# Kernel optimization log

Hardware: AMD Instinct MI355X
Metric: run time of the kernel (lower is better)

The kernel has to match this reference:

```python
import jax, jax.numpy as jnp
import numpy as np

N, E, F_IN, HID, HEADS, OUT, G = 50000, 800000, 128, 64, 4, 10, 64
NEG_SLOPE = 0.2


def _glorot(key, shape):
    fan = shape[0] + shape[-1]
    lim = np.sqrt(6.0 / fan)
    return jax.random.uniform(key, shape, jnp.float32, -lim, lim)


def setup_inputs() -> dict:
    key = jax.random.key(0)
    ks = jax.random.split(key, 20)
    x = jax.random.normal(ks[0], (N, F_IN), jnp.float32)
    edge_index = jax.random.randint(ks[1], (2, E), 0, N, jnp.int64)
    batch = jnp.sort(jax.random.randint(ks[2], (N,), 0, G, jnp.int64))
    inp = {"x": x, "edge_index": edge_index, "batch": batch}
    # layer 1: in=F_IN, heads=HEADS, out=HID
    inp["W1"] = _glorot(ks[3], (F_IN, HEADS * HID))
    inp["b1"] = jnp.zeros((HEADS * HID,), jnp.float32)
    inp["as1"] = _glorot(ks[4], (HEADS, HID))
    inp["ad1"] = _glorot(ks[5], (HEADS, HID))
    # layer 2: in=HEADS*HID, heads=HEADS, out=HID
    inp["W2"] = _glorot(ks[6], (HEADS * HID, HEADS * HID))
    inp["b2"] = jnp.zeros((HEADS * HID,), jnp.float32)
    inp["as2"] = _glorot(ks[7], (HEADS, HID))
    inp["ad2"] = _glorot(ks[8], (HEADS, HID))
    # layer 3: in=HEADS*HID, heads=1, out=HID
    inp["W3"] = _glorot(ks[9], (HEADS * HID, HID))
    inp["b3"] = jnp.zeros((HID,), jnp.float32)
    inp["as3"] = _glorot(ks[10], (1, HID))
    inp["ad3"] = _glorot(ks[11], (1, HID))
    # MLP head [HID, HID, OUT]
    inp["Wm1"] = _glorot(ks[12], (HID, HID))
    inp["bm1"] = jnp.zeros((HID,), jnp.float32)
    inp["Wm2"] = _glorot(ks[13], (HID, OUT))
    inp["bm2"] = jnp.zeros((OUT,), jnp.float32)
    return inp


def _gat_layer(x, src, dst, W, b, att_src, att_dst):
    # x: [N, Fin]; att_*: [H, C]
    H, C = att_src.shape
    h = (x @ W).reshape(N, H, C)
    a_src = jnp.einsum("nhc,hc->nh", h, att_src)
    a_dst = jnp.einsum("nhc,hc->nh", h, att_dst)
    alpha = jax.nn.leaky_relu(a_src[src] + a_dst[dst], NEG_SLOPE)  # [E', H]
    amax = jax.ops.segment_max(alpha, dst, num_segments=N)
    alpha = jnp.exp(alpha - amax[dst])
    denom = jax.ops.segment_sum(alpha, dst, num_segments=N)
    alpha = alpha / (denom[dst] + 1e-16)
    msg = h[src] * alpha[:, :, None]  # [E', H, C]
    out = jax.ops.segment_sum(msg, dst, num_segments=N)  # [N, H, C]
    return out.reshape(N, H * C) + b


def reference(x, edge_index, batch, W1, b1, as1, ad1, W2, b2, as2, ad2, W3, b3, as3, ad3, Wm1, bm1, Wm2, bm2):
    # PyG GATConv adds self-loops by default
    loops = jnp.arange(N, dtype=edge_index.dtype)
    src = jnp.concatenate([edge_index[0], loops])
    dst = jnp.concatenate([edge_index[1], loops])
    h = jax.nn.relu(_gat_layer(x, src, dst, W1, b1, as1, ad1))
    h = jax.nn.relu(_gat_layer(h, src, dst, W2, b2, as2, ad2))
    h = jax.nn.relu(_gat_layer(h, src, dst, W3, b3, as3, ad3))
    pooled = jax.ops.segment_sum(h, batch, num_segments=G)  # [G, HID]
    hidden = jax.nn.relu(pooled @ Wm1 + bm1)
    return hidden @ Wm2 + bm2
```

## Files before the change

### kernel.cpp

```cpp
#include <hip/hip_runtime.h>
#include <hip/hip_bf16.h>

#define F_IN   128
#define HID    64
#define HEADS  4
#define OUTD   10
#define NGRP   64

typedef unsigned short u16;
typedef __attribute__((ext_vector_type(8))) short short8;
typedef __attribute__((ext_vector_type(4))) float f32x4;

__device__ __forceinline__ float atomAddF(float* p, float v) {
    return __hip_atomic_fetch_add(p, v, __ATOMIC_RELAXED, __HIP_MEMORY_SCOPE_AGENT);
}
__device__ __forceinline__ float lrelu(float f) { return f > 0.f ? f : 0.2f * f; }
__device__ __forceinline__ float b2f(u16 u) { return __uint_as_float(((unsigned)u) << 16); }
__device__ __forceinline__ u16 f2b(float f) {
    unsigned u = __float_as_uint(f);
    return (u16)((u + 0x7fffu + ((u >> 16) & 1u)) >> 16);
}
__device__ __forceinline__ unsigned fmono(float f) {
    unsigned u = __float_as_uint(f);
    return (u & 0x80000000u) ? ~u : (u | 0x80000000u);
}
__device__ __forceinline__ float funmono(unsigned u) {
    return __uint_as_float((u & 0x80000000u) ? (u & 0x7FFFFFFFu) : ~u);
}

__global__ __launch_bounds__(256) void conv_kernel(const float* __restrict__ in,
                                                   u16* __restrict__ out, int n4) {
    int i = blockIdx.x * 256 + threadIdx.x;
    if (i >= n4) return;
    float4 v = ((const float4*)in)[i];
    uint2 o;
    o.x = (unsigned)f2b(v.x) | ((unsigned)f2b(v.y) << 16);
    o.y = (unsigned)f2b(v.z) | ((unsigned)f2b(v.w) << 16);
    ((uint2*)out)[i] = o;
}

__global__ __launch_bounds__(256) void wtrans_kernel(const float* __restrict__ W,
                                                     u16* __restrict__ Wt, int K, int NC) {
    int i = blockIdx.x * 256 + threadIdx.x;
    if (i >= K * NC) return;
    int n = i / K, k = i - n * K;
    Wt[i] = f2b(W[(size_t)k * NC + n]);
}

template<int K, int NC>
__global__ __launch_bounds__(256) void gemm_bf16_kernel(const u16* __restrict__ A,
                                                        const u16* __restrict__ Bt,
                                                        u16* __restrict__ Hb, int nrows) {
    constexpr int LDA = 40;
    __shared__ u16 As[64][LDA];
    __shared__ u16 Bs[NC][LDA];
    int tid = threadIdx.x;
    int m0 = blockIdx.x * 64;
    int w = tid >> 6, l = tid & 63, lr = l & 15, lk = l >> 4;
    if constexpr (NC == 256) {
        f32x4 acc[4][4] = {};
        for (int k0 = 0; k0 < K; k0 += 32) {
            {
                int row = tid >> 2, ks = (tid & 3) * 8;
                int grow = m0 + row;
                short8 av = {};
                if (grow < nrows) av = *(const short8*)&A[(size_t)grow * K + k0 + ks];
                *(short8*)&As[row][ks] = av;
            }
            #pragma unroll
            for (int i = 0; i < 4; i++) {
                int col = (tid >> 2) + 64 * i;
                int ks = (tid & 3) * 8;
                *(short8*)&Bs[col][ks] = *(const short8*)&Bt[(size_t)col * K + k0 + ks];
            }
            __syncthreads();
            short8 a[4], b[4];
            #pragma unroll
            for (int mi = 0; mi < 4; mi++) a[mi] = *(const short8*)&As[16 * mi + lr][lk * 8];
            #pragma unroll
            for (int ni = 0; ni < 4; ni++) b[ni] = *(const short8*)&Bs[64 * w + 16 * ni + lr][lk * 8];
            #pragma unroll
            for (int mi = 0; mi < 4; mi++)
                #pragma unroll
                for (int ni = 0; ni < 4; ni++)
                    acc[mi][ni] = __builtin_amdgcn_mfma_f32_16x16x32_bf16(a[mi], b[ni], acc[mi][ni], 0, 0, 0);
            __syncthreads();
        }
        #pragma unroll
        for (int mi = 0; mi < 4; mi++) {
            #pragma unroll
            for (int j = 0; j < 4; j++) {
                int grow = m0 + 16 * mi + lk * 4 + j;
                if (grow < nrows) {
                    #pragma unroll
                    for (int ni = 0; ni < 4; ni++)
                        Hb[(size_t)grow * NC + 64 * w + 16 * ni + lr] = f2b(acc[mi][ni][j]);
                }
            }
        }
    } else {
        f32x4 acc[NC / 16] = {};
        for (int k0 = 0; k0 < K; k0 += 32) {
            {
                int row = tid >> 2, ks = (tid & 3) * 8;
                int grow = m0 + row;
                short8 av = {};
                if (grow < nrows) av = *(const short8*)&A[(size_t)grow * K + k0 + ks];
                *(short8*)&As[row][ks] = av;
            }
            {
                int col = tid >> 2;
                int ks = (tid & 3) * 8;
                if (col < NC) *(short8*)&Bs[col][ks] = *(const short8*)&Bt[(size_t)col * K + k0 + ks];
            }
            __syncthreads();
            short8 af = *(const short8*)&As[16 * w + lr][lk * 8];
            #pragma unroll
            for (int c = 0; c < NC / 16; c++) {
                short8 bf = *(const short8*)&Bs[c * 16 + lr][lk * 8];
                acc[c] = __builtin_amdgcn_mfma_f32_16x16x32_bf16(af, bf, acc[c], 0, 0, 0);
            }
            __syncthreads();
        }
        #pragma unroll
        for (int c = 0; c < NC / 16; c++) {
            #pragma unroll
            for (int j = 0; j < 4; j++) {
                int grow = m0 + 16 * w + lk * 4 + j;
                if (grow < nrows) Hb[(size_t)grow * NC + c * 16 + lr] = f2b(acc[c][j]);
            }
        }
    }
}

template<int HH>
__global__ __launch_bounds__(256) void att_kernel(const u16* __restrict__ Hm,
                                                  const float* __restrict__ as_,
                                                  const float* __restrict__ ad_,
                                                  float* __restrict__ a_src,
                                                  float* __restrict__ a_dst, int n_nodes) {
    int wave = (blockIdx.x * 256 + threadIdx.x) >> 6;
    int lane = threadIdx.x & 63;
    if (wave >= n_nodes) return;
    const u16* hrow = Hm + (size_t)wave * HH * 64;
    #pragma unroll
    for (int hh = 0; hh < HH; hh++) {
        float v = b2f(hrow[hh * 64 + lane]);
        float s = v * as_[hh * 64 + lane];
        float d = v * ad_[hh * 64 + lane];
        #pragma unroll
        for (int off = 32; off; off >>= 1) {
            s += __shfl_xor(s, off, 64);
            d += __shfl_xor(d, off, 64);
        }
        if (lane == 0) { a_src[wave * HH + hh] = s; a_dst[wave * HH + hh] = d; }
    }
}

template<int HH>
__global__ __launch_bounds__(256) void gmax_kernel(const float* __restrict__ a_src,
                                                   unsigned* __restrict__ gmaxu, int n_nodes) {
    float mx[HH];
    #pragma unroll
    for (int h = 0; h < HH; h++) mx[h] = -3.4e38f;
    for (int i = blockIdx.x * 256 + threadIdx.x; i < n_nodes; i += gridDim.x * 256) {
        #pragma unroll
        for (int h = 0; h < HH; h++) mx[h] = fmaxf(mx[h], a_src[i * HH + h]);
    }
    #pragma unroll
    for (int h = 0; h < HH; h++) {
        #pragma unroll
        for (int off = 32; off; off >>= 1) mx[h] = fmaxf(mx[h], __shfl_xor(mx[h], off, 64));
    }
    if ((threadIdx.x & 63) == 0) {
        #pragma unroll
        for (int h = 0; h < HH; h++) atomicMax(&gmaxu[h], fmono(mx[h]));
    }
}

__global__ void count_kernel(const int* __restrict__ ei, int* __restrict__ deg,
                             int E_, int n_nodes) {
    int e = blockIdx.x * 256 + threadIdx.x;
    int tot = E_ + n_nodes;
    if (e >= tot) return;
    int d = (e < E_) ? ei[E_ + e] : e - E_;
    atomicAdd(&deg[d], 1);
}

__global__ __launch_bounds__(256) void scan_reduce_kernel(const int* __restrict__ deg,
                                                          int* __restrict__ bsum, int n) {
    int i = blockIdx.x * 256 + threadIdx.x;
    int v = (i < n) ? deg[i] : 0;
    #pragma unroll
    for (int o = 32; o; o >>= 1) v += __shfl_xor(v, o, 64);
    __shared__ int ws[4];
    if ((threadIdx.x & 63) == 0) ws[threadIdx.x >> 6] = v;
    __syncthreads();
    if (threadIdx.x == 0) bsum[blockIdx.x] = ws[0] + ws[1] + ws[2] + ws[3];
}

__global__ __launch_bounds__(256) void scan_blocksums_kernel(int* __restrict__ bsum, int nb) {
    __shared__ int s[256];
    int t = threadIdx.x;
    int v = (t < nb) ? bsum[t] : 0;
    s[t] = v;
    __syncthreads();
    #pragma unroll
    for (int d = 1; d < 256; d <<= 1) {
        int x = (t >= d) ? s[t - d] : 0;
        __syncthreads();
        s[t] += x;
        __syncthreads();
    }
    if (t < nb) bsum[t] = s[t] - v;
}

__global__ __launch_bounds__(256) void scan_final_kernel(const int* __restrict__ deg,
                                                         const int* __restrict__ bsum,
                                                         int* __restrict__ off, int n) {
    __shared__ int s[256];
    int t = threadIdx.x;
    int i = blockIdx.x * 256 + t;
    int v = (i < n) ? deg[i] : 0;
    s[t] = v;
    __syncthreads();
    #pragma unroll
    for (int d = 1; d < 256; d <<= 1) {
        int x = (t >= d) ? s[t - d] : 0;
        __syncthreads();
        s[t] += x;
        __syncthreads();
    }
    int ex = s[t] - v + bsum[blockIdx.x];
    if (i < n) off[i] = ex;
    if (i == n - 1) off[n] = ex + v;
}

__global__ void fill_kernel(const int* __restrict__ ei, const int* __restrict__ off,
                            int* __restrict__ cursor, int* __restrict__ csr_src,
                            int E_, int n_nodes) {
    int e = blockIdx.x * 256 + threadIdx.x;
    int tot = E_ + n_nodes;
    if (e >= tot) return;
    int s, d;
    if (e < E_) { s = ei[e]; d = ei[E_ + e]; } else { s = d = e - E_; }
    int pos = atomicAdd(&cursor[d], 1);
    csr_src[off[d] + pos] = s;
}

template<int HH, int CPL, bool OUTF32>
__global__ __launch_bounds__(256) void gat_aggr_kernel(const int* __restrict__ off,
                                                       const int* __restrict__ csr_src,
                                                       const u16* __restrict__ Hb,
                                                       const float* __restrict__ a_src,
                                                       const float* __restrict__ a_dst,
                                                       const unsigned* __restrict__ gmaxu,
                                                       const float* __restrict__ bias,
                                                       u16* __restrict__ outb16,
                                                       float* __restrict__ outf32,
                                                       int n_nodes) {
    constexpr int HC = 64 * CPL;
    constexpr int GRP = 64 / HH;
    int d = blockIdx.x * 4 + (threadIdx.x >> 6);
    if (d >= n_nodes) return;
    int lane = threadIdx.x & 63;
    int hh = lane / GRP;
    int g = lane & (GRP - 1);
    int gb = lane & (64 - GRP);
    int o0 = off[d];
    int deg = off[d + 1] - o0;
    float adm = a_dst[d * HH + hh];
    float m = lrelu(funmono(gmaxu[hh]) + adm);

    float den = 0.f;
    float acc[CPL] = {};
    int j = 0;
    for (; j + 4 <= deg; j += 4) {
        int s0 = csr_src[o0 + j + 0];
        int s1 = csr_src[o0 + j + 1];
        int s2 = csr_src[o0 + j + 2];
        int s3 = csr_src[o0 + j + 3];
        int ssel = s3;
        if (g == 0) ssel = s0; else if (g == 1) ssel = s1; else if (g == 2) ssel = s2;
        float e = __expf(lrelu(a_src[ssel * HH + hh] + adm) - m);
        float e0 = __shfl(e, gb + 0, 64);
        float e1 = __shfl(e, gb + 1, 64);
        float e2 = __shfl(e, gb + 2, 64);
        float e3 = __shfl(e, gb + 3, 64);
        den += (e0 + e1) + (e2 + e3);
        if constexpr (CPL == 4) {
            uint2 h0 = *(const uint2*)&Hb[(size_t)s0 * HC + lane * 4];
            uint2 h1 = *(const uint2*)&Hb[(size_t)s1 * HC + lane * 4];
            uint2 h2 = *(const uint2*)&Hb[(size_t)s2 * HC + lane * 4];
            uint2 h3 = *(const uint2*)&Hb[(size_t)s3 * HC + lane * 4];
            acc[0] += e0 * __uint_as_float(h0.x << 16) + e1 * __uint_as_float(h1.x << 16)
                    + e2 * __uint_as_float(h2.x << 16) + e3 * __uint_as_float(h3.x << 16);
            acc[1] += e0 * __uint_as_float(h0.x & 0xffff0000u) + e1 * __uint_as_float(h1.x & 0xffff0000u)
                    + e2 * __uint_as_float(h2.x & 0xffff0000u) + e3 * __uint_as_float(h3.x & 0xffff0000u);
            acc[2] += e0 * __uint_as_float(h0.y << 16) + e1 * __uint_as_float(h1.y << 16)
                    + e2 * __uint_as_float(h2.y << 16) + e3 * __uint_as_float(h3.y << 16);
            acc[3] += e0 * __uint_as_float(h0.y & 0xffff0000u) + e1 * __uint_as_float(h1.y & 0xffff0000u)
                    + e2 * __uint_as_float(h2.y & 0xffff0000u) + e3 * __uint_as_float(h3.y & 0xffff0000u);
        } else {
            u16 h0 = Hb[(size_t)s0 * HC + lane];
            u16 h1 = Hb[(size_t)s1 * HC + lane];
            u16 h2 = Hb[(size_t)s2 * HC + lane];
            u16 h3 = Hb[(size_t)s3 * HC + lane];
            acc[0] += e0 * b2f(h0) + e1 * b2f(h1) + e2 * b2f(h2) + e3 * b2f(h3);
        }
    }
    for (; j < deg; j++) {
        int s = csr_src[o0 + j];
        float al = __expf(lrelu(a_src[s * HH + hh] + adm) - m);
        den += al;
        if constexpr (CPL == 4) {
            uint2 hv = *(const uint2*)&Hb[(size_t)s * HC + lane * 4];
            acc[0] += al * __uint_as_float(hv.x << 16);
            acc[1] += al * __uint_as_float(hv.x & 0xffff0000u);
            acc[2] += al * __uint_as_float(hv.y << 16);
            acc[3] += al * __uint_as_float(hv.y & 0xffff0000u);
        } else {
            acc[0] += al * b2f(Hb[(size_t)s * HC + lane]);
        }
    }
    float inv = 1.f / (den + 1e-16f);
    if constexpr (CPL == 4) {
        float4 bv = *(const float4*)&bias[lane * 4];
        float v0 = fmaxf(acc[0] * inv + bv.x, 0.f);
        float v1 = fmaxf(acc[1] * inv + bv.y, 0.f);
        float v2 = fmaxf(acc[2] * inv + bv.z, 0.f);
        float v3 = fmaxf(acc[3] * inv + bv.w, 0.f);
        uint2 o;
        o.x = (unsigned)f2b(v0) | ((unsigned)f2b(v1) << 16);
        o.y = (unsigned)f2b(v2) | ((unsigned)f2b(v3) << 16);
        *(uint2*)&outb16[(size_t)d * HC + lane * 4] = o;
    } else {
        float v = fmaxf(acc[0] * inv + bias[lane], 0.f);
        if constexpr (OUTF32) outf32[(size_t)d * HC + lane] = v;
        else                  outb16[(size_t)d * HC + lane] = f2b(v);
    }
}

__global__ __launch_bounds__(256) void pool_kernel(const float* __restrict__ H3,
                                                   const int* __restrict__ batch,
                                                   float* __restrict__ pooled, int n_nodes) {
    int wave = (blockIdx.x * 256 + threadIdx.x) >> 6;
    int lane = threadIdx.x & 63;
    int nwaves = gridDim.x * 4;
    int chunk = (n_nodes + nwaves - 1) / nwaves;
    int start = wave * chunk;
    int end = min(n_nodes, start + chunk);
    if (start >= end) return;
    int cur = batch[start];
    float acc = 0.f;
    for (int n = start; n < end; n++) {
        int g = batch[n];
        if (g != cur) { atomAddF(&pooled[cur * 64 + lane], acc); acc = 0.f; cur = g; }
        acc += H3[(size_t)n * 64 + lane];
    }
    atomAddF(&pooled[cur * 64 + lane], acc);
}

__global__ __launch_bounds__(64) void mlp_kernel(const float* __restrict__ pooled,
                                                 const float* __restrict__ Wm1,
                                                 const float* __restrict__ bm1,
                                                 const float* __restrict__ Wm2,
                                                 const float* __restrict__ bm2,
                                                 float* __restrict__ out) {
    __shared__ float sp[64], sh[64];
    int g = blockIdx.x, t = threadIdx.x;
    sp[t] = pooled[g * 64 + t];
    __syncthreads();
    float a = bm1[t];
    for (int k = 0; k < 64; k++) a += sp[k] * Wm1[k * 64 + t];
    sh[t] = a > 0.f ? a : 0.f;
    __syncthreads();
    if (t < 10) {
        float o = bm2[t];
        for (int j = 0; j < 64; j++) o += sh[j] * Wm2[j * 10 + t];
        out[g * 10 + t] = o;
    }
}

extern "C" void kernel_launch(void* const* d_in, const int* in_sizes, int n_in,
                              void* d_out, int out_size, void* d_ws, size_t ws_size,
                              hipStream_t stream) {
    const float* x   = (const float*)d_in[0];
    const int*   ei  = (const int*)d_in[1];
    const int*   bat = (const int*)d_in[2];
    const float* W1  = (const float*)d_in[3];
    const float* b1  = (const float*)d_in[4];
    const float* as1 = (const float*)d_in[5];
    const float* ad1 = (const float*)d_in[6];
    const float* W2  = (const float*)d_in[7];
    const float* b2  = (const float*)d_in[8];
    const float* as2 = (const float*)d_in[9];
    const float* ad2 = (const float*)d_in[10];
    const float* W3  = (const float*)d_in[11];
    const float* b3  = (const float*)d_in[12];
    const float* as3 = (const float*)d_in[13];
    const float* ad3 = (const float*)d_in[14];
    const float* Wm1 = (const float*)d_in[15];
    const float* bm1 = (const float*)d_in[16];
    const float* Wm2 = (const float*)d_in[17];
    const float* bm2 = (const float*)d_in[18];
    float* out = (float*)d_out;

    const int Nn = in_sizes[0] / F_IN;
    const int Ee = in_sizes[1] / 2;
    const int Et = Ee + Nn;

    char* wsp = (char*)d_ws;
    size_t off_b = 0;
    auto alloc = [&](size_t bytes) { void* p = wsp + off_b; off_b += (bytes + 255) & ~(size_t)255; return p; };
    u16*   xb      = (u16*)alloc((size_t)Nn * F_IN * 2);
    u16*   HbA     = (u16*)alloc((size_t)Nn * 256 * 2);
    u16*   HbB     = (u16*)alloc((size_t)Nn * 256 * 2);
    float* Hf      = (float*)alloc((size_t)Nn * HID * 4);
    u16*   Wt1     = (u16*)alloc((size_t)256 * 128 * 2);
    u16*   Wt2     = (u16*)alloc((size_t)256 * 256 * 2);
    u16*   Wt3     = (u16*)alloc((size_t)64 * 256 * 2);
    float* a_src   = (float*)alloc((size_t)Nn * HEADS * 4);
    float* a_dst   = (float*)alloc((size_t)Nn * HEADS * 4);
    unsigned* gmaxu = (unsigned*)alloc(16 * 4);
    int*   deg     = (int*)alloc((size_t)Nn * 2 * 4);
    int*   cursor  = deg + Nn;
    int*   bsum    = (int*)alloc((size_t)256 * 4);
    int*   csr_off = (int*)alloc((size_t)(Nn + 1) * 4);
    int*   csr_src = (int*)alloc((size_t)Et * 4);
    float* pooled  = (float*)alloc((size_t)NGRP * HID * 4);
    (void)ws_size;

    int n4 = Nn * F_IN / 4;
    conv_kernel<<<(n4 + 255) / 256, 256, 0, stream>>>(x, xb, n4);
    wtrans_kernel<<<(128 * 256 + 255) / 256, 256, 0, stream>>>(W1, Wt1, 128, 256);
    wtrans_kernel<<<(256 * 256 + 255) / 256, 256, 0, stream>>>(W2, Wt2, 256, 256);
    wtrans_kernel<<<(256 * 64 + 255) / 256, 256, 0, stream>>>(W3, Wt3, 256, 64);

    hipMemsetAsync(deg, 0, (size_t)Nn * 2 * 4, stream);
    hipMemsetAsync(gmaxu, 0, 16 * 4, stream);
    int eb = (Et + 255) / 256;
    int nb = (Nn + 255) / 256;
    count_kernel<<<eb, 256, 0, stream>>>(ei, deg, Ee, Nn);
    scan_reduce_kernel<<<nb, 256, 0, stream>>>(deg, bsum, Nn);
    scan_blocksums_kernel<<<1, 256, 0, stream>>>(bsum, nb);
    scan_final_kernel<<<nb, 256, 0, stream>>>(deg, bsum, csr_off, Nn);
    fill_kernel<<<eb, 256, 0, stream>>>(ei, csr_off, cursor, csr_src, Ee, Nn);

    const int gemm_blocks = (Nn + 63) / 64;
    const int nodeBlocks = (Nn + 3) / 4;

    gemm_bf16_kernel<128, 256><<<gemm_blocks, 256, 0, stream>>>(xb, Wt1, HbA, Nn);
    att_kernel<4><<<nodeBlocks, 256, 0, stream>>>(HbA, as1, ad1, a_src, a_dst, Nn);
    gmax_kernel<4><<<64, 256, 0, stream>>>(a_src, gmaxu + 0, Nn);
    gat_aggr_kernel<4, 4, false><<<nodeBlocks, 256, 0, stream>>>(csr_off, csr_src, HbA,
                                                                 a_src, a_dst, gmaxu + 0, b1,
                                                                 HbB, nullptr, Nn);
    gemm_bf16_kernel<256, 256><<<gemm_blocks, 256, 0, stream>>>(HbB, Wt2, HbA, Nn);
    att_kernel<4><<<nodeBlocks, 256, 0, stream>>>(HbA, as2, ad2, a_src, a_dst, Nn);
    gmax_kernel<4><<<64, 256, 0, stream>>>(a_src, gmaxu + 4, Nn);
    gat_aggr_kernel<4, 4, false><<<nodeBlocks, 256, 0, stream>>>(csr_off, csr_src, HbA,
                                                                 a_src, a_dst, gmaxu + 4, b2,
                                                                 HbB, nullptr, Nn);
    gemm_bf16_kernel<256, 64><<<gemm_blocks, 256, 0, stream>>>(HbB, Wt3, HbA, Nn);
    att_kernel<1><<<nodeBlocks, 256, 0, stream>>>(HbA, as3, ad3, a_src, a_dst, Nn);
    gmax_kernel<1><<<64, 256, 0, stream>>>(a_src, gmaxu + 8, Nn);
    gat_aggr_kernel<1, 1, true><<<nodeBlocks, 256, 0, stream>>>(csr_off, csr_src, HbA,
                                                                a_src, a_dst, gmaxu + 8, b3,
                                                                nullptr, Hf, Nn);

    hipMemsetAsync(pooled, 0, (size_t)NGRP * HID * 4, stream);
    pool_kernel<<<128, 256, 0, stream>>>(Hf, bat, pooled, Nn);
    mlp_kernel<<<NGRP, 64, 0, stream>>>(pooled, Wm1, bm1, Wm2, bm2, out);
}
```

Before: 456.7 us.

## Fuse attention scores and input conversion into GEMMs, unroll aggregation by eight

The attention-score dot products are now computed in the GEMM epilogue from the fp32 accumulators, which removes the separate att_kernel passes that re-read H. Layer 1 loads fp32 x and converts it to bf16 inside the GEMM, so the conversion kernel and the bf16 copy of x are gone. The three weight-transpose launches are merged into one. The edge aggregation loop now processes 8 neighbours per step instead of 4 to expose more memory-level parallelism. The trade-off is higher register pressure in both the GEMM epilogue and the aggregation kernel. Attention scores are also now taken from fp32 accumulators rather than from bf16-rounded H.

```diff
diff --git a/kernel.cpp b/kernel.cpp
--- a/kernel.cpp
+++ b/kernel.cpp
@@ -28,35 +28,44 @@
     return __uint_as_float((u & 0x80000000u) ? (u & 0x7FFFFFFFu) : ~u);
 }
 
-__global__ __launch_bounds__(256) void conv_kernel(const float* __restrict__ in,
-                                                   u16* __restrict__ out, int n4) {
+__global__ __launch_bounds__(256) void wtrans_all_kernel(const float* __restrict__ W1,
+                                                         const float* __restrict__ W2,
+                                                         const float* __restrict__ W3,
+                                                         u16* __restrict__ Wt1,
+                                                         u16* __restrict__ Wt2,
+                                                         u16* __restrict__ Wt3) {
     int i = blockIdx.x * 256 + threadIdx.x;
-    if (i >= n4) return;
-    float4 v = ((const float4*)in)[i];
-    uint2 o;
-    o.x = (unsigned)f2b(v.x) | ((unsigned)f2b(v.y) << 16);
-    o.y = (unsigned)f2b(v.z) | ((unsigned)f2b(v.w) << 16);
-    ((uint2*)out)[i] = o;
-}
-
-__global__ __launch_bounds__(256) void wtrans_kernel(const float* __restrict__ W,
-                                                     u16* __restrict__ Wt, int K, int NC) {
-    int i = blockIdx.x * 256 + threadIdx.x;
-    if (i >= K * NC) return;
-    int n = i / K, k = i - n * K;
-    Wt[i] = f2b(W[(size_t)k * NC + n]);
-}
-
-template<int K, int NC>
-__global__ __launch_bounds__(256) void gemm_bf16_kernel(const u16* __restrict__ A,
-                                                        const u16* __restrict__ Bt,
-                                                        u16* __restrict__ Hb, int nrows) {
+    if (i < 32768) {
+        int n = i >> 7, k = i & 127;
+        Wt1[i] = f2b(W1[(size_t)k * 256 + n]);
+    } else if (i < 98304) {
+        int j = i - 32768;
+        int n = j >> 8, k = j & 255;
+        Wt2[j] = f2b(W2[(size_t)k * 256 + n]);
+    } else if (i < 114688) {
+        int j = i - 98304;
+        int n = j >> 8, k = j & 255;
+        Wt3[j] = f2b(W3[(size_t)k * 64 + n]);
+    }
+}
+
+template<int K, int NC, bool AF32>
+__global__ __launch_bounds__(256) void gemm_att_kernel(const void* __restrict__ Aptr,
+                                                       const u16* __restrict__ Bt,
+                                                       const float* __restrict__ as_,
+                                                       const float* __restrict__ ad_,
+                                                       u16* __restrict__ Hb,
+                                                       float* __restrict__ a_src,
+                                                       float* __restrict__ a_dst,
+                                                       int nrows) {
     constexpr int LDA = 40;
+    constexpr int HH = NC / 64;
     __shared__ u16 As[64][LDA];
     __shared__ u16 Bs[NC][LDA];
     int tid = threadIdx.x;
     int m0 = blockIdx.x * 64;
     int w = tid >> 6, l = tid & 63, lr = l & 15, lk = l >> 4;
+
     if constexpr (NC == 256) {
         f32x4 acc[4][4] = {};
         for (int k0 = 0; k0 < K; k0 += 32) {
@@ -64,7 +73,19 @@
                 int row = tid >> 2, ks = (tid & 3) * 8;
                 int grow = m0 + row;
                 short8 av = {};
-                if (grow < nrows) av = *(const short8*)&A[(size_t)grow * K + k0 + ks];
+                if (grow < nrows) {
+                    if constexpr (AF32) {
+                        const float* src = (const float*)Aptr + (size_t)grow * K + k0 + ks;
+                        float4 v0 = *(const float4*)src;
+                        float4 v1 = *(const float4*)(src + 4);
+                        av[0] = (short)f2b(v0.x); av[1] = (short)f2b(v0.y);
+                        av[2] = (short)f2b(v0.z); av[3] = (short)f2b(v0.w);
+                        av[4] = (short)f2b(v1.x); av[5] = (short)f2b(v1.y);
+                        av[6] = (short)f2b(v1.z); av[7] = (short)f2b(v1.w);
+                    } else {
+                        av = *(const short8*)&((const u16*)Aptr)[(size_t)grow * K + k0 + ks];
+                    }
+                }
                 *(short8*)&As[row][ks] = av;
             }
             #pragma unroll
@@ -98,62 +119,93 @@
                 }
             }
         }
+        float asv[4], adv[4];
+        #pragma unroll
+        for (int ni = 0; ni < 4; ni++) {
+            asv[ni] = as_[w * 64 + 16 * ni + lr];
+            adv[ni] = ad_[w * 64 + 16 * ni + lr];
+        }
+        #pragma unroll
+        for (int mi = 0; mi < 4; mi++) {
+            #pragma unroll
+            for (int j = 0; j < 4; j++) {
+                float ps = 0.f, pd = 0.f;
+                #pragma unroll
+                for (int ni = 0; ni < 4; ni++) {
+                    float v = acc[mi][ni][j];
+                    ps += v * asv[ni];
+                    pd += v * adv[ni];
+                }
+                #pragma unroll
+                for (int o = 1; o < 16; o <<= 1) {
+                    ps += __shfl_xor(ps, o, 64);
+                    pd += __shfl_xor(pd, o, 64);
+                }
+                int grow = m0 + 16 * mi + lk * 4 + j;
+                if (lr == 0 && grow < nrows) {
+                    a_src[grow * HH + w] = ps;
+                    a_dst[grow * HH + w] = pd;
+                }
+            }
+        }
     } else {
-        f32x4 acc[NC / 16] = {};
+        f32x4 acc[4] = {};
         for (int k0 = 0; k0 < K; k0 += 32) {
             {
                 int row = tid >> 2, ks = (tid & 3) * 8;
                 int grow = m0 + row;
                 short8 av = {};
-                if (grow < nrows) av = *(const short8*)&A[(size_t)grow * K + k0 + ks];
+                if (grow < nrows) av = *(const short8*)&((const u16*)Aptr)[(size_t)grow * K + k0 + ks];
                 *(short8*)&As[row][ks] = av;
             }
             {
                 int col = tid >> 2;
                 int ks = (tid & 3) * 8;
-                if (col < NC) *(short8*)&Bs[col][ks] = *(const short8*)&Bt[(size_t)col * K + k0 + ks];
+                *(short8*)&Bs[col][ks] = *(const short8*)&Bt[(size_t)col * K + k0 + ks];
             }
             __syncthreads();
             short8 af = *(const short8*)&As[16 * w + lr][lk * 8];
             #pragma unroll
-            for (int c = 0; c < NC / 16; c++) {
+            for (int c = 0; c < 4; c++) {
                 short8 bf = *(const short8*)&Bs[c * 16 + lr][lk * 8];
                 acc[c] = __builtin_amdgcn_mfma_f32_16x16x32_bf16(af, bf, acc[c], 0, 0, 0);
             }
             __syncthreads();
         }
         #pragma unroll
-        for (int c = 0; c < NC / 16; c++) {
+        for (int c = 0; c < 4; c++) {
             #pragma unroll
             for (int j = 0; j < 4; j++) {
                 int grow = m0 + 16 * w + lk * 4 + j;
                 if (grow < nrows) Hb[(size_t)grow * NC + c * 16 + lr] = f2b(acc[c][j]);
             }
         }
-    }
-}
-
-template<int HH>
-__global__ __launch_bounds__(256) void att_kernel(const u16* __restrict__ Hm,
-                                                  const float* __restrict__ as_,
-                                                  const float* __restrict__ ad_,
-                                                  float* __restrict__ a_src,
-                                                  float* __restrict__ a_dst, int n_nodes) {
-    int wave = (blockIdx.x * 256 + threadIdx.x) >> 6;
-    int lane = threadIdx.x & 63;
-    if (wave >= n_nodes) return;
-    const u16* hrow = Hm + (size_t)wave * HH * 64;
-    #pragma unroll
-    for (int hh = 0; hh < HH; hh++) {
-        float v = b2f(hrow[hh * 64 + lane]);
-        float s = v * as_[hh * 64 + lane];
-        float d = v * ad_[hh * 64 + lane];
-        #pragma unroll
-        for (int off = 32; off; off >>= 1) {
-            s += __shfl_xor(s, off, 64);
-            d += __shfl_xor(d, off, 64);
-        }
-        if (lane == 0) { a_src[wave * HH + hh] = s; a_dst[wave * HH + hh] = d; }
+        float asv[4], adv[4];
+        #pragma unroll
+        for (int c = 0; c < 4; c++) {
+            asv[c] = as_[c * 16 + lr];
+            adv[c] = ad_[c * 16 + lr];
+        }
+        #pragma unroll
+        for (int j = 0; j < 4; j++) {
+            float ps = 0.f, pd = 0.f;
+            #pragma unroll
+            for (int c = 0; c < 4; c++) {
+                float v = acc[c][j];
+                ps += v * asv[c];
+                pd += v * adv[c];
+            }
+            #pragma unroll
+            for (int o = 1; o < 16; o <<= 1) {
+                ps += __shfl_xor(ps, o, 64);
+                pd += __shfl_xor(pd, o, 64);
+            }
+            int grow = m0 + 16 * w + lk * 4 + j;
+            if (lr == 0 && grow < nrows) {
+                a_src[grow] = ps;
+                a_dst[grow] = pd;
+            }
+        }
     }
 }
 
@@ -275,38 +327,34 @@
     float den = 0.f;
     float acc[CPL] = {};
     int j = 0;
-    for (; j + 4 <= deg; j += 4) {
-        int s0 = csr_src[o0 + j + 0];
-        int s1 = csr_src[o0 + j + 1];
-        int s2 = csr_src[o0 + j + 2];
-        int s3 = csr_src[o0 + j + 3];
-        int ssel = s3;
-        if (g == 0) ssel = s0; else if (g == 1) ssel = s1; else if (g == 2) ssel = s2;
+    for (; j + 8 <= deg; j += 8) {
+        int s[8];
+        #pragma unroll
+        for (int t = 0; t < 8; t++) s[t] = csr_src[o0 + j + t];
+        int ssel = s[g & 7];
         float e = __expf(lrelu(a_src[ssel * HH + hh] + adm) - m);
-        float e0 = __shfl(e, gb + 0, 64);
-        float e1 = __shfl(e, gb + 1, 64);
-        float e2 = __shfl(e, gb + 2, 64);
-        float e3 = __shfl(e, gb + 3, 64);
-        den += (e0 + e1) + (e2 + e3);
+        float ee[8];
+        #pragma unroll
+        for (int t = 0; t < 8; t++) ee[t] = __shfl(e, gb + t, 64);
+        #pragma unroll
+        for (int t = 0; t < 8; t++) den += ee[t];
         if constexpr (CPL == 4) {
-            uint2 h0 = *(const uint2*)&Hb[(size_t)s0 * HC + lane * 4];
-            uint2 h1 = *(const uint2*)&Hb[(size_t)s1 * HC + lane * 4];
-            uint2 h2 = *(const uint2*)&Hb[(size_t)s2 * HC + lane * 4];
-            uint2 h3 = *(const uint2*)&Hb[(size_t)s3 * HC + lane * 4];
-            acc[0] += e0 * __uint_as_float(h0.x << 16) + e1 * __uint_as_float(h1.x << 16)
-                    + e2 * __uint_as_float(h2.x << 16) + e3 * __uint_as_float(h3.x << 16);
-            acc[1] += e0 * __uint_as_float(h0.x & 0xffff0000u) + e1 * __uint_as_float(h1.x & 0xffff0000u)
-                    + e2 * __uint_as_float(h2.x & 0xffff0000u) + e3 * __uint_as_float(h3.x & 0xffff0000u);
-            acc[2] += e0 * __uint_as_float(h0.y << 16) + e1 * __uint_as_float(h1.y << 16)
-                    + e2 * __uint_as_float(h2.y << 16) + e3 * __uint_as_float(h3.y << 16);
-            acc[3] += e0 * __uint_as_float(h0.y & 0xffff0000u) + e1 * __uint_as_float(h1.y & 0xffff0000u)
-                    + e2 * __uint_as_float(h2.y & 0xffff0000u) + e3 * __uint_as_float(h3.y & 0xffff0000u);
+            uint2 hv[8];
+            #pragma unroll
+            for (int t = 0; t < 8; t++) hv[t] = *(const uint2*)&Hb[(size_t)s[t] * HC + lane * 4];
+            #pragma unroll
+            for (int t = 0; t < 8; t++) {
+                acc[0] += ee[t] * __uint_as_float(hv[t].x << 16);
+                acc[1] += ee[t] * __uint_as_float(hv[t].x & 0xffff0000u);
+                acc[2] += ee[t] * __uint_as_float(hv[t].y << 16);
+                acc[3] += ee[t] * __uint_as_float(hv[t].y & 0xffff0000u);
+            }
         } else {
-            u16 h0 = Hb[(size_t)s0 * HC + lane];
-            u16 h1 = Hb[(size_t)s1 * HC + lane];
-            u16 h2 = Hb[(size_t)s2 * HC + lane];
-            u16 h3 = Hb[(size_t)s3 * HC + lane];
-            acc[0] += e0 * b2f(h0) + e1 * b2f(h1) + e2 * b2f(h2) + e3 * b2f(h3);
+            u16 hv[8];
+            #pragma unroll
+            for (int t = 0; t < 8; t++) hv[t] = Hb[(size_t)s[t] * HC + lane];
+            #pragma unroll
+            for (int t = 0; t < 8; t++) acc[0] += ee[t] * b2f(hv[t]);
         }
     }
     for (; j < deg; j++) {
@@ -413,7 +461,6 @@
     char* wsp = (char*)d_ws;
     size_t off_b = 0;
     auto alloc = [&](size_t bytes) { void* p = wsp + off_b; off_b += (bytes + 255) & ~(size_t)255; return p; };
-    u16*   xb      = (u16*)alloc((size_t)Nn * F_IN * 2);
     u16*   HbA     = (u16*)alloc((size_t)Nn * 256 * 2);
     u16*   HbB     = (u16*)alloc((size_t)Nn * 256 * 2);
     float* Hf      = (float*)alloc((size_t)Nn * HID * 4);
@@ -431,11 +478,7 @@
     float* pooled  = (float*)alloc((size_t)NGRP * HID * 4);
     (void)ws_size;
 
-    int n4 = Nn * F_IN / 4;
-    conv_kernel<<<(n4 + 255) / 256, 256, 0, stream>>>(x, xb, n4);
-    wtrans_kernel<<<(128 * 256 + 255) / 256, 256, 0, stream>>>(W1, Wt1, 128, 256);
-    wtrans_kernel<<<(256 * 256 + 255) / 256, 256, 0, stream>>>(W2, Wt2, 256, 256);
-    wtrans_kernel<<<(256 * 64 + 255) / 256, 256, 0, stream>>>(W3, Wt3, 256, 64);
+    wtrans_all_kernel<<<(114688 + 255) / 256, 256, 0, stream>>>(W1, W2, W3, Wt1, Wt2, Wt3);
 
     hipMemsetAsync(deg, 0, (size_t)Nn * 2 * 4, stream);
     hipMemsetAsync(gmaxu, 0, 16 * 4, stream);
@@ -450,20 +493,20 @@
     const int gemm_blocks = (Nn + 63) / 64;
     const int nodeBlocks = (Nn + 3) / 4;
 
-    gemm_bf16_kernel<128, 256><<<gemm_blocks, 256, 0, stream>>>(xb, Wt1, HbA, Nn);
-    att_kernel<4><<<nodeBlocks, 256, 0, stream>>>(HbA, as1, ad1, a_src, a_dst, Nn);
+    gemm_att_kernel<128, 256, true><<<gemm_blocks, 256, 0, stream>>>(x, Wt1, as1, ad1,
+                                                                     HbA, a_src, a_dst, Nn);
     gmax_kernel<4><<<64, 256, 0, stream>>>(a_src, gmaxu + 0, Nn);
     gat_aggr_kernel<4, 4, false><<<nodeBlocks, 256, 0, stream>>>(csr_off, csr_src, HbA,
                                                                  a_src, a_dst, gmaxu + 0, b1,
                                                                  HbB, nullptr, Nn);
-    gemm_bf16_kernel<256, 256><<<gemm_blocks, 256, 0, stream>>>(HbB, Wt2, HbA, Nn);
-    att_kernel<4><<<nodeBlocks, 256, 0, stream>>>(HbA, as2, ad2, a_src, a_dst, Nn);
+    gemm_att_kernel<256, 256, false><<<gemm_blocks, 256, 0, stream>>>(HbB, Wt2, as2, ad2,
+                                                                      HbA, a_src, a_dst, Nn);
     gmax_kernel<4><<<64, 256, 0, stream>>>(a_src, gmaxu + 4, Nn);
     gat_aggr_kernel<4, 4, false><<<nodeBlocks, 256, 0, stream>>>(csr_off, csr_src, HbA,
                                                                  a_src, a_dst, gmaxu + 4, b2,
                                                                  HbB, nullptr, Nn);
-    gemm_bf16_kernel<256, 64><<<gemm_blocks, 256, 0, stream>>>(HbB, Wt3, HbA, Nn);
-    att_kernel<1><<<nodeBlocks, 256, 0, stream>>>(HbA, as3, ad3, a_src, a_dst, Nn);
+    gemm_att_kernel<256, 64, false><<<gemm_blocks, 256, 0, stream>>>(HbB, Wt3, as3, ad3,
+                                                                     HbA, a_src, a_dst, Nn);
     gmax_kernel<1><<<64, 256, 0, stream>>>(a_src, gmaxu + 8, Nn);
     gat_aggr_kernel<1, 1, true><<<nodeBlocks, 256, 0, stream>>>(csr_off, csr_src, HbA,
                                                                 a_src, a_dst, gmaxu + 8, b3,
```

New measurement: 406.0 us. -11.1%, faster.
